# Kernel optimization log

Hardware: AMD Instinct MI355X
Metric: run time of the kernel (lower is better)

The kernel has to match this reference:

```python
import jax, jax.numpy as jnp
import numpy as np

HIDDEN = 4096       # in_features of gate/up proj
INTER = 11008       # intermediate_size (per projection)
GROUP = 128         # GPTQ group size
B, S = 4, 2048
NIB = jnp.uint32(0xF)


def _pack_rows(nib):
    """Pack 4-bit values along rows: [8*R, C] uint32 -> [R, C] uint32."""
    r = nib.reshape(-1, 8, nib.shape[-1])
    shifts = (jnp.arange(8, dtype=jnp.uint32) * 4)[None, :, None]
    return jnp.sum(r << shifts, axis=1, dtype=jnp.uint32)  # disjoint bits -> sum == OR


def _pack_cols(nib):
    """Pack 4-bit values along cols: [G, 8*C] uint32 -> [G, C] uint32."""
    r = nib.reshape(nib.shape[0], -1, 8)
    shifts = (jnp.arange(8, dtype=jnp.uint32) * 4)[None, None, :]
    return jnp.sum(r << shifts, axis=2, dtype=jnp.uint32)


def setup_inputs() -> dict:
    key = jax.random.key(0)
    ks = jax.random.split(key, 7)
    n_groups = HIDDEN // GROUP          # 32 groups for gate_up
    n_groups_d = INTER // GROUP         # 86 groups for down

    x = jax.random.normal(ks[0], (B, S, HIDDEN), jnp.float32)

    # gate_up_proj: in=HIDDEN, out=2*INTER
    nib_w_gu = jax.random.randint(ks[1], (HIDDEN, 2 * INTER), 0, 16).astype(jnp.uint32)
    nib_z_gu = jax.random.randint(ks[2], (n_groups, 2 * INTER), 0, 15).astype(jnp.uint32)
    qweight_gu = _pack_rows(nib_w_gu)                          # [HIDDEN//8, 2*INTER]
    qzeros_gu = _pack_cols(nib_z_gu)                           # [n_groups, 2*INTER//8]
    scales_gu = jax.random.uniform(ks[3], (n_groups, 2 * INTER), jnp.float32, 0.005, 0.02)
    g_idx_gu = (jnp.arange(HIDDEN, dtype=jnp.int32) // GROUP)

    # down_proj: in=INTER, out=HIDDEN
    nib_w_d = jax.random.randint(ks[4], (INTER, HIDDEN), 0, 16).astype(jnp.uint32)
    nib_z_d = jax.random.randint(ks[5], (n_groups_d, HIDDEN), 0, 15).astype(jnp.uint32)
    qweight_down = _pack_rows(nib_w_d)                         # [INTER//8, HIDDEN]
    qzeros_down = _pack_cols(nib_z_d)                          # [n_groups_d, HIDDEN//8]
    scales_down = jax.random.uniform(ks[6], (n_groups_d, HIDDEN), jnp.float32, 0.005, 0.02)
    g_idx_down = (jnp.arange(INTER, dtype=jnp.int32) // GROUP)

    return {
        "x": x,
        "qweight_gu": qweight_gu, "qzeros_gu": qzeros_gu,
        "scales_gu": scales_gu, "g_idx_gu": g_idx_gu,
        "qweight_down": qweight_down, "qzeros_down": qzeros_down,
        "scales_down": scales_down, "g_idx_down": g_idx_down,
    }


def _dequant(qw, qz, sc, g_idx):
    """GPTQ v2 dequant: W[i,j] = sc[g[i],j] * (wq[i,j] - (zq[g[i],j] + 1))."""
    shifts = jnp.arange(8, dtype=jnp.uint32) * 4
    # unpack qweight along rows: [R, C] -> [8*R, C]
    wq = ((qw[:, None, :] >> shifts[None, :, None]) & NIB)
    wq = wq.reshape(-1, qw.shape[1]).astype(jnp.float32)
    # unpack qzeros along cols: [G, C//8] -> [G, C]; +1 per GPTQ v2 convention
    zq = ((qz[:, :, None] >> shifts[None, None, :]) & NIB)
    zq = zq.reshape(qz.shape[0], -1).astype(jnp.float32) + 1.0
    return sc[g_idx] * (wq - zq[g_idx])  # [in, out]


def reference(x, qweight_gu, qzeros_gu, scales_gu, g_idx_gu,
              qweight_down, qzeros_down, scales_down, g_idx_down):
    w_gu = _dequant(qweight_gu, qzeros_gu, scales_gu, g_idx_gu)          # [HIDDEN, 2*INTER]
    inter = jnp.einsum('bsh,hf->bsf', x, w_gu)                            # [B,S,2*INTER]
    gate, up = inter[..., :INTER], inter[..., INTER:]
    h = jax.nn.silu(gate) * up                                            # SwiGLU
    w_d = _dequant(qweight_down, qzeros_down, scales_down, g_idx_down)   # [INTER, HIDDEN]
    return jnp.einsum('bsf,fh->bsh', h, w_d)
```

## Files before the change

kernel.cpp:

```cpp
#include <hip/hip_runtime.h>
#include <stdint.h>

#define HIDDEN 4096
#define INTER  11008
#define NTOK   8192
#define WROW   22016

typedef __bf16 bf16;
typedef __bf16 bf16x8 __attribute__((ext_vector_type(8)));
typedef _Float16 f16;
typedef _Float16 f16x2 __attribute__((ext_vector_type(2)));
typedef _Float16 f16x8 __attribute__((ext_vector_type(8)));
typedef float  f32x4  __attribute__((ext_vector_type(4)));
typedef unsigned int u32x4 __attribute__((ext_vector_type(4)));

__device__ __forceinline__ void gload16(const void* g, void* l) {
  __builtin_amdgcn_global_load_lds(
      (const __attribute__((address_space(1))) void*)g,
      (__attribute__((address_space(3))) void*)l, 16, 0, 0);
}
__device__ __forceinline__ void gload4(const void* g, void* l) {
  __builtin_amdgcn_global_load_lds(
      (const __attribute__((address_space(1))) void*)g,
      (__attribute__((address_space(3))) void*)l, 4, 0, 0);
}

__global__ __launch_bounds__(256) void cvt_f16_kernel(const float* __restrict__ x,
                                                      f16* __restrict__ y) {
  const int i = (blockIdx.x * 256 + threadIdx.x) * 8;
  f32x4 a = *(const f32x4*)(x + i);
  f32x4 b = *(const f32x4*)(x + i + 4);
  f16x8 v;
#pragma unroll
  for (int j = 0; j < 4; ++j) { v[2 * j] = (f16)a[j]; v[2 * j + 1] = (f16)b[j]; }
  *(f16x8*)(y + i) = v;
}

__global__ __launch_bounds__(256) void spak_kernel(const uint32_t* __restrict__ qz,
                                                   const float* __restrict__ sc,
                                                   uint32_t* __restrict__ outp) {
  const int idx = blockIdx.x * 256 + threadIdx.x;
  const int gq = idx / WROW;
  const int n = idx - gq * WROW;
  const int grp = n >> 5, win = n & 31;
  const int jg = (win < 16) ? grp * 16 + win : INTER + grp * 16 + (win - 16);
  const float s = sc[(size_t)gq * WROW + jg];
  const uint32_t z = (qz[(size_t)gq * (WROW / 8) + (jg >> 3)] >> ((jg & 7) * 4)) & 15u;
  union { f16 h[2]; uint32_t u; } a, b;
  a.h[0] = (f16)s; a.h[1] = (f16)s;
  b.h[0] = (f16)(float)(1025u + z); b.h[1] = b.h[0];
  outp[(size_t)idx * 2 + 0] = a.u;
  outp[(size_t)idx * 2 + 1] = b.u;
}

__global__ __launch_bounds__(256) void repackB_kernel(const uint32_t* __restrict__ qw,
                                                      uint32_t* __restrict__ outp) {
  const size_t idx = (size_t)blockIdx.x * 256 + threadIdx.x;
  const int c = (int)(idx & 2047);
  const int kt = (int)((idx >> 11) & 63);
  const int nb = (int)(idx >> 17);
  const int j = c & 3;
  const int chunk = c >> 2;
  const int r = chunk >> 6;
  const int wc = (chunk >> 4) & 3;
  const int fr = chunk & 15;
  const int col = wc * 32 + fr + (j & 1) * 16 + (j >> 1) * 128;
  const int n = nb * 256 + col;
  const int grp = n >> 5, win = n & 31;
  const int jg = (win < 16) ? grp * 16 + win : INTER + grp * 16 + (win - 16);
  outp[idx] = qw[(size_t)(kt * 8 + r) * WROW + jg];
}

__global__ __launch_bounds__(256) void dequant_kernel(const uint32_t* __restrict__ qw,
                                                      const uint32_t* __restrict__ qz,
                                                      const float* __restrict__ sc,
                                                      bf16* __restrict__ out,
                                                      int J, int Kout) {
  __shared__ __align__(16) bf16 T[64 * 256];
  const int tid = threadIdx.x;
  const int tx = tid & 63, ty = tid >> 6;
  const int j0 = blockIdx.x * 64, r0 = blockIdx.y * 32;
  const int j = j0 + tx;
  const int J8 = J >> 3;
#pragma unroll
  for (int i = 0; i < 8; ++i) {
    const int r = r0 + ty * 8 + i;
    const int g = r >> 4;
    const uint32_t w = qw[(size_t)r * J + j];
    const float s = sc[(size_t)g * J + j];
    const uint32_t zb = (qz[(size_t)g * J8 + (j >> 3)] >> ((j & 7) * 4)) & 15u;
    const float zoff = (float)(zb + 1u);
    bf16x8 v;
#pragma unroll
    for (int e = 0; e < 8; ++e) {
      const float wv = (float)((w >> (e * 4)) & 15u);
      v[e] = (bf16)(s * (wv - zoff));
    }
    const int lb = (tx * 512 + (ty * 8 + i) * 16) ^ ((tx & 31) << 4);
    *(bf16x8*)((char*)T + lb) = v;
  }
  __syncthreads();
#pragma unroll
  for (int u = 0; u < 8; ++u) {
    const int unit = u * 256 + tid;
    const int jj = unit >> 5;
    const int ob = (unit & 31) * 16;
    const int lb = (jj * 512 + ob) ^ ((jj & 31) << 4);
    bf16x8 v = *(const bf16x8*)((const char*)T + lb);
    *(bf16x8*)(out + (size_t)(j0 + jj) * Kout + r0 * 8 + (ob >> 1)) = v;
  }
}

#define OFF_BP 65536
#define OFF_SPK 81920

#define BAR __builtin_amdgcn_s_barrier()
#define LGKM0                                              \
  do {                                                     \
    asm volatile("s_waitcnt lgkmcnt(0)" ::: "memory");     \
    __builtin_amdgcn_sched_barrier(0);                     \
  } while (0)
#define VM2 asm volatile("s_waitcnt vmcnt(2)" ::: "memory")
#define VM3 asm volatile("s_waitcnt vmcnt(3)" ::: "memory")

#define STG_A(buf, h, tt)                                                      \
  do {                                                                         \
    gload16(sA00 + ((size_t)((h) * 128) * (HIDDEN * 2)) + (size_t)(tt) * 128,  \
            lds + (buf) * 32768 + (h) * 16384 + w * 1024);                     \
    gload16(sA00 + ((size_t)((h) * 128 + 64) * (HIDDEN * 2)) + (size_t)(tt) * 128, \
            lds + (buf) * 32768 + (h) * 16384 + 8192 + w * 1024);              \
  } while (0)

#define STG_B(buf, tt)                                                         \
  gload16(repk_src + (size_t)(tt) * 2048 + tid * 4,                            \
          lds + OFF_BP + (buf) * 8192 + tid * 16)

#define STG_SPK(gt)                                                           \
  gload4(spakg + ((size_t)(gt) * WROW + n0) * 2 + tid,                        \
         lds + OFF_SPK + ((gt) & 3) * 2048 + w * 256)

__device__ __forceinline__ f16x8 unpack8s(uint32_t u, f16x2 s2, f16x2 k2) {
  const uint32_t MSK = 0x000F000Fu, M = 0x64006400u;
  uint32_t q0 = (u & MSK) | M;
  uint32_t q1 = ((u >> 4) & MSK) | M;
  uint32_t q2 = ((u >> 8) & MSK) | M;
  uint32_t q3 = ((u >> 12) & MSK) | M;
  f16x2 w0 = (__builtin_bit_cast(f16x2, q0) - k2) * s2;
  f16x2 w1 = (__builtin_bit_cast(f16x2, q1) - k2) * s2;
  f16x2 w2 = (__builtin_bit_cast(f16x2, q2) - k2) * s2;
  f16x2 w3 = (__builtin_bit_cast(f16x2, q3) - k2) * s2;
  f16x8 r;
  r[0] = w0[0]; r[1] = w0[1]; r[2] = w1[0]; r[3] = w1[1];
  r[4] = w2[0]; r[5] = w2[1]; r[6] = w3[0]; r[7] = w3[1];
  return r;
}

#define UNP_SL(AVH, BUIDX, NH, NJ, KK, R, C)                                   \
  do {                                                                         \
    bv[NJ][KK] = unpack8s(bu[BUIDX], s2r[NH][NJ], k2r[NH][NJ]);                \
    _Pragma("unroll") for (int mi = 0; mi < 4; ++mi)                           \
      acc[(R) + mi][C] = __builtin_amdgcn_mfma_f32_16x16x32_f16(               \
          AVH[mi][KK], bv[NJ][KK], acc[(R) + mi][C], 0, 0, 0);                 \
  } while (0)

#define MFMA16(AVH, R, CBASE)                                                  \
  do {                                                                         \
    _Pragma("unroll") for (int kk = 0; kk < 2; ++kk)                           \
      _Pragma("unroll") for (int nj = 0; nj < 2; ++nj)                         \
        _Pragma("unroll") for (int mi = 0; mi < 4; ++mi)                       \
          acc[(R) + mi][(CBASE) + nj] = __builtin_amdgcn_mfma_f32_16x16x32_f16(\
              AVH[mi][kk], bv[nj][kk], acc[(R) + mi][(CBASE) + nj], 0, 0, 0);  \
  } while (0)

__global__ __launch_bounds__(512, 2) void gemm1q(const f16* __restrict__ A,
                                                 const uint32_t* __restrict__ repk,
                                                 const uint32_t* __restrict__ spakg,
                                                 bf16* __restrict__ H) {
  extern __shared__ char lds[];
  const int tid = threadIdx.x;
  const int lane = tid & 63, w = tid >> 6;
  const int wr = w >> 2, wc = w & 3;
  const int fr = lane & 15, fg = lane >> 4;
  constexpr int NT = HIDDEN / 64;

  const int wg = blockIdx.x;
  const int nb = wg % (WROW / 256), mb = wg / (WROW / 256);
  const int m0 = mb << 8, n0 = nb << 8;

  const int rbase = tid >> 3;
  const int cbyte0 = (tid & 7) * 16;
  const int cL0 = cbyte0 ^ ((rbase & 7) << 4);
  const char* sA00 = (const char*)A + (size_t)(m0 + rbase) * (size_t)(HIDDEN * 2) + cL0;

  const uint32_t* repk_src = repk + (size_t)nb * 64 * 2048;

  const int swz = (fr & 7) << 4;
  const int ck[2] = {(fg * 16) ^ swz, (64 + fg * 16) ^ swz};
  const int aro = (wr * 64 + fr) * 128;
  auto lda = [&](int buf, int mh, int mi, int kk) -> f16x8 {
    return *(const f16x8*)(lds + buf * 32768 + mh * 16384 + aro + mi * 2048 + ck[kk]);
  };
  const int c1b = ((fg * 4 + wc) * 16 + fr) * 16;
  const int ncol[2][2] = {{wc * 32 + fr, wc * 32 + 16 + fr},
                          {wc * 32 + 128 + fr, wc * 32 + 144 + fr}};

  f32x4 acc[8][4];
#pragma unroll
  for (int i = 0; i < 8; ++i)
#pragma unroll
    for (int j = 0; j < 4; ++j) acc[i][j] = (f32x4)0.0f;
  f16x8 av0[4][2], av1[4][2], bv[2][2];
  uint32_t bu[8];
  f16x2 s2r[2][2], k2r[2][2];

  STG_SPK(0);
  STG_A(0, 0, 0);
  STG_B(0, 0);
  STG_A(0, 1, 0);
  VM2;
  BAR;

  for (int t = 0; t < NT; ++t) {
    const int cb = t & 1, nx = cb ^ 1, g = t >> 1;
    const int t1 = (t + 1 < NT) ? t + 1 : 0;

#pragma unroll
    for (int mi = 0; mi < 4; ++mi) { av0[mi][0] = lda(cb, 0, mi, 0); av0[mi][1] = lda(cb, 0, mi, 1); }
    {
      u32x4 v1 = *(const u32x4*)(lds + OFF_BP + cb * 8192 + c1b);
      u32x4 v2 = *(const u32x4*)(lds + OFF_BP + cb * 8192 + c1b + 4096);
      bu[0] = v1.x; bu[1] = v2.x; bu[2] = v1.y; bu[3] = v2.y;
      bu[4] = v1.z; bu[5] = v2.z; bu[6] = v1.w; bu[7] = v2.w;
    }
    if ((t & 1) == 0) {
      const char* sp = lds + OFF_SPK + (g & 3) * 2048;
#pragma unroll
      for (int nh = 0; nh < 2; ++nh)
#pragma unroll
        for (int nj = 0; nj < 2; ++nj) {
          s2r[nh][nj] = *(const f16x2*)(sp + ncol[nh][nj] * 8);
          k2r[nh][nj] = *(const f16x2*)(sp + ncol[nh][nj] * 8 + 4);
        }
    }
    STG_A(nx, 0, t1);
    STG_B(nx, t1);
    VM3;
    BAR; LGKM0;
    __builtin_amdgcn_s_setprio(1);
    UNP_SL(av0, 0, 0, 0, 0, 0, 0);
    UNP_SL(av0, 1, 0, 0, 1, 0, 0);
    UNP_SL(av0, 2, 0, 1, 0, 0, 1);
    UNP_SL(av0, 3, 0, 1, 1, 0, 1);
    __builtin_amdgcn_s_setprio(0);
    __builtin_amdgcn_sched_barrier(0);
    BAR;

#pragma unroll
    for (int mi = 0; mi < 4; ++mi) { av1[mi][0] = lda(cb, 1, mi, 0); av1[mi][1] = lda(cb, 1, mi, 1); }
    if (t & 1) {
      const int gt = (g + 1 < 32) ? g + 1 : 31;
      STG_SPK(gt);
    }
    STG_A(nx, 1, t1);
    BAR; LGKM0;
    __builtin_amdgcn_s_setprio(1);
    MFMA16(av1, 4, 0);
    __builtin_amdgcn_s_setprio(0);
    __builtin_amdgcn_sched_barrier(0);
    BAR;

    __builtin_amdgcn_s_setprio(1);
    UNP_SL(av1, 4, 1, 0, 0, 4, 2);
    UNP_SL(av1, 5, 1, 0, 1, 4, 2);
    UNP_SL(av1, 6, 1, 1, 0, 4, 3);
    UNP_SL(av1, 7, 1, 1, 1, 4, 3);
    MFMA16(av0, 0, 2);
    __builtin_amdgcn_s_setprio(0);
    __builtin_amdgcn_sched_barrier(0);
    VM2;
    BAR;
  }
  asm volatile("s_waitcnt vmcnt(0)" ::: "memory");

#pragma unroll
  for (int mh = 0; mh < 2; ++mh)
#pragma unroll
    for (int mi = 0; mi < 4; ++mi)
#pragma unroll
      for (int nh = 0; nh < 2; ++nh) {
        const f32x4 gv4 = acc[mh * 4 + mi][nh * 2];
        const f32x4 uv4 = acc[mh * 4 + mi][nh * 2 + 1];
        const int col = (n0 >> 1) + wc * 16 + nh * 64 + fr;
#pragma unroll
        for (int rr = 0; rr < 4; ++rr) {
          const int row = m0 + wr * 64 + mh * 128 + mi * 16 + fg * 4 + rr;
          const float gv = gv4[rr], uv = uv4[rr];
          H[(size_t)row * INTER + col] = (bf16)(gv / (1.0f + __expf(-gv)) * uv);
        }
      }
}

#define OFF_A2 0
#define OFF_B2 32768

#define STG2(mat, buf, h, t)                                                   \
  do {                                                                         \
    gload16(s##mat[h][0] + (size_t)(t) * 128,                                  \
            lds + (buf) * 65536 + OFF_##mat + (h) * 16384 + w * 1024);         \
    gload16(s##mat[h][1] + (size_t)(t) * 128,                                  \
            lds + (buf) * 65536 + OFF_##mat + (h) * 16384 + 8192 + w * 1024);  \
  } while (0)
#define VM6 asm volatile("s_waitcnt vmcnt(6)" ::: "memory")

#define MFMA_Q2(MH, NH)                                                        \
  do {                                                                         \
    __builtin_amdgcn_s_setprio(1);                                             \
    _Pragma("unroll") for (int kk = 0; kk < 2; ++kk) {                         \
      _Pragma("unroll") for (int nj = 0; nj < 2; ++nj) {                       \
        _Pragma("unroll") for (int mi = 0; mi < 4; ++mi) {                     \
          acc[(MH)*4 + mi][(NH)*2 + nj] = __builtin_amdgcn_mfma_f32_16x16x32_bf16( \
              av[mi][kk], bv[nj][kk], acc[(MH)*4 + mi][(NH)*2 + nj], 0, 0, 0); \
        }                                                                      \
      }                                                                        \
    }                                                                          \
    __builtin_amdgcn_s_setprio(0);                                             \
    __builtin_amdgcn_sched_barrier(0);                                         \
  } while (0)

template <int K, int NT, int NNB>
__global__ __launch_bounds__(512, 2) void gemm8p(const bf16* __restrict__ A,
                                                 const bf16* __restrict__ Bm,
                                                 float* __restrict__ O) {
  extern __shared__ char lds[];
  const int tid = threadIdx.x;
  const int lane = tid & 63, w = tid >> 6;
  const int wr = w >> 2, wc = w & 3;
  const int fr = lane & 15, fg = lane >> 4;

  const int wg = blockIdx.x;
  const int nb = wg % NNB, mb = wg / NNB;
  const int m0 = mb << 8, n0 = nb << 8;

  const char* sA2[2][2];
  const char* sB2[2][2];
#pragma unroll
  for (int h = 0; h < 2; ++h)
#pragma unroll
    for (int l = 0; l < 2; ++l) {
      const int d = h * 16384 + (l * 512 + tid) * 16;
      const int r = d >> 7;
      const int cL = (d & 127) ^ ((r & 7) << 4);
      sA2[h][l] = (const char*)A + (size_t)(m0 + r) * (size_t)(K * 2) + cL;
      sB2[h][l] = (const char*)Bm + (size_t)(n0 + r) * (size_t)(K * 2) + cL;
    }

  const int swz = (fr & 7) << 4;
  const int ck[2] = {(fg * 16) ^ swz, (64 + fg * 16) ^ swz};
  const int aro = (wr * 64 + fr) * 128;
  const int bro = OFF_B2 + (wc * 32 + fr) * 128;

  auto lda = [&](int buf, int mh, int mi, int kk) -> bf16x8 {
    return *(const bf16x8*)(lds + buf * 65536 + mh * 16384 + aro + mi * 2048 + ck[kk]);
  };
  auto ldb = [&](int buf, int nh, int nj, int kk) -> bf16x8 {
    return *(const bf16x8*)(lds + buf * 65536 + bro + nh * 16384 + nj * 2048 + ck[kk]);
  };

  f32x4 acc[8][4];
#pragma unroll
  for (int i = 0; i < 8; ++i)
#pragma unroll
    for (int j = 0; j < 4; ++j) acc[i][j] = (f32x4)0.0f;
  bf16x8 av[4][2], bv[2][2];

  STG2(A2, 0, 0, 0);
  STG2(B2, 0, 0, 0);
  STG2(B2, 0, 1, 0);
  STG2(A2, 0, 1, 0);
  STG2(A2, 1, 0, 1);
  STG2(B2, 1, 1, 1);
  STG2(A2, 1, 1, 1);
  VM6;
  BAR;

  for (int t = 0; t < NT; ++t) {
    const int cb = t & 1, nx = cb ^ 1;
    const int t1 = (t + 1 < NT) ? t + 1 : 0;
    const int t2 = (t + 2 < NT) ? t + 2 : 0;

#pragma unroll
    for (int mi = 0; mi < 4; ++mi) { av[mi][0] = lda(cb, 0, mi, 0); av[mi][1] = lda(cb, 0, mi, 1); }
#pragma unroll
    for (int nj = 0; nj < 2; ++nj) { bv[nj][0] = ldb(cb, 0, nj, 0); bv[nj][1] = ldb(cb, 0, nj, 1); }
    STG2(B2, nx, 0, t1);
    BAR; LGKM0;
    MFMA_Q2(0, 0);
    BAR;

#pragma unroll
    for (int nj = 0; nj < 2; ++nj) { bv[nj][0] = ldb(cb, 1, nj, 0); bv[nj][1] = ldb(cb, 1, nj, 1); }
    STG2(A2, cb, 0, t2);
    BAR; LGKM0;
    MFMA_Q2(0, 1);
    BAR;

#pragma unroll
    for (int mi = 0; mi < 4; ++mi) { av[mi][0] = lda(cb, 1, mi, 0); av[mi][1] = lda(cb, 1, mi, 1); }
    STG2(B2, cb, 1, t2);
    BAR; LGKM0;
    MFMA_Q2(1, 1);
    BAR;

#pragma unroll
    for (int nj = 0; nj < 2; ++nj) { bv[nj][0] = ldb(cb, 0, nj, 0); bv[nj][1] = ldb(cb, 0, nj, 1); }
    STG2(A2, cb, 1, t2);
    VM6;
    BAR; LGKM0;
    MFMA_Q2(1, 0);
    BAR;
  }

#pragma unroll
  for (int mh = 0; mh < 2; ++mh)
#pragma unroll
    for (int mi = 0; mi < 4; ++mi)
#pragma unroll
      for (int nh = 0; nh < 2; ++nh)
#pragma unroll
        for (int nj = 0; nj < 2; ++nj) {
          const f32x4 a = acc[mh * 4 + mi][nh * 2 + nj];
          const int col = n0 + wc * 32 + nh * 128 + nj * 16 + fr;
#pragma unroll
          for (int rr = 0; rr < 4; ++rr) {
            const int row = m0 + wr * 64 + mh * 128 + mi * 16 + fg * 4 + rr;
            __builtin_nontemporal_store(a[rr], &O[(size_t)row * HIDDEN + col]);
          }
        }
}

extern "C" void kernel_launch(void* const* d_in, const int* in_sizes, int n_in,
                              void* d_out, int out_size, void* d_ws, size_t ws_size,
                              hipStream_t stream) {
  (void)in_sizes; (void)n_in; (void)out_size; (void)ws_size;
  const float*    x     = (const float*)d_in[0];
  const uint32_t* qw_gu = (const uint32_t*)d_in[1];
  const uint32_t* qz_gu = (const uint32_t*)d_in[2];
  const float*    sc_gu = (const float*)d_in[3];
  const uint32_t* qw_d  = (const uint32_t*)d_in[5];
  const uint32_t* qz_d  = (const uint32_t*)d_in[6];
  const float*    sc_d  = (const float*)d_in[7];
  float*          out   = (float*)d_out;

  char* ws = (char*)d_ws;
  const size_t XB  = (size_t)NTOK * HIDDEN * 2;
  const size_t W2B = (size_t)HIDDEN * INTER * 2;
  const size_t HB  = (size_t)NTOK * INTER * 2;
  const size_t SPB = (size_t)32 * WROW * 2 * 4;
  f16*      xb    = (f16*)ws;
  bf16*     wt    = (bf16*)(ws + XB);
  bf16*     hb    = (bf16*)(ws + XB + W2B);
  uint32_t* spakg = (uint32_t*)(ws + XB + W2B + HB);
  uint32_t* repk  = (uint32_t*)(ws + XB + W2B + HB + SPB);

  hipFuncSetAttribute((const void*)&gemm1q,
                      hipFuncAttributeMaxDynamicSharedMemorySize, 90112);
  hipFuncSetAttribute((const void*)&gemm8p<INTER, INTER / 64, HIDDEN / 256>,
                      hipFuncAttributeMaxDynamicSharedMemorySize, 131072);

  cvt_f16_kernel<<<NTOK * HIDDEN / 2048, 256, 0, stream>>>(x, xb);
  spak_kernel<<<32 * WROW / 256, 256, 0, stream>>>(qz_gu, sc_gu, spakg);
  repackB_kernel<<<((WROW / 256) * 64 * 2048) / 256, 256, 0, stream>>>(qw_gu, repk);

  gemm1q<<<(WROW / 256) * (NTOK / 256), 512, 90112, stream>>>(xb, repk, spakg, hb);

  dequant_kernel<<<dim3(HIDDEN / 64, (INTER / 8) / 32), 256, 0, stream>>>(
      qw_d, qz_d, sc_d, wt, HIDDEN, INTER);
  gemm8p<INTER, INTER / 64, HIDDEN / 256>
      <<<(HIDDEN / 256) * (NTOK / 256), 512, 131072, stream>>>(hb, wt, out);
}
```

Baseline: 2.113 ms.

## Restructure gemm1q inner loop to dequantize all B fragments up front and share one A register set

The per-tile schedule is reorganized so all eight B words are dequantized in the first phase against the first A half. The second A half then reuses the same av registers for all remaining MFMAs, which merges the last two phases into one and drops one barrier per iteration. This removes the separate av0/av1 and bu register arrays, lowering register pressure under the 512x2 launch bounds. In exchange, dequant work is no longer interleaved across phases, which may reduce overlap with MFMA, and more B fragment registers stay live.

```diff
diff --git a/kernel.cpp b/kernel.cpp
--- a/kernel.cpp
+++ b/kernel.cpp
@@ -155,21 +155,12 @@
   return r;
 }
 
-#define UNP_SL(AVH, BUIDX, NH, NJ, KK, R, C)                                   \
+#define UNP_SL(BV, WORD, NH, NJ, KK, C)                                        \
   do {                                                                         \
-    bv[NJ][KK] = unpack8s(bu[BUIDX], s2r[NH][NJ], k2r[NH][NJ]);                \
+    BV[NJ][KK] = unpack8s(WORD, s2r[NH][NJ], k2r[NH][NJ]);                     \
     _Pragma("unroll") for (int mi = 0; mi < 4; ++mi)                           \
-      acc[(R) + mi][C] = __builtin_amdgcn_mfma_f32_16x16x32_f16(               \
-          AVH[mi][KK], bv[NJ][KK], acc[(R) + mi][C], 0, 0, 0);                 \
-  } while (0)
-
-#define MFMA16(AVH, R, CBASE)                                                  \
-  do {                                                                         \
-    _Pragma("unroll") for (int kk = 0; kk < 2; ++kk)                           \
-      _Pragma("unroll") for (int nj = 0; nj < 2; ++nj)                         \
-        _Pragma("unroll") for (int mi = 0; mi < 4; ++mi)                       \
-          acc[(R) + mi][(CBASE) + nj] = __builtin_amdgcn_mfma_f32_16x16x32_f16(\
-              AVH[mi][kk], bv[nj][kk], acc[(R) + mi][(CBASE) + nj], 0, 0, 0);  \
+      acc[mi][C] = __builtin_amdgcn_mfma_f32_16x16x32_f16(                     \
+          av[mi][KK], BV[NJ][KK], acc[mi][C], 0, 0, 0);                        \
   } while (0)
 
 __global__ __launch_bounds__(512, 2) void gemm1q(const f16* __restrict__ A,
@@ -209,8 +200,7 @@
   for (int i = 0; i < 8; ++i)
 #pragma unroll
     for (int j = 0; j < 4; ++j) acc[i][j] = (f32x4)0.0f;
-  f16x8 av0[4][2], av1[4][2], bv[2][2];
-  uint32_t bu[8];
+  f16x8 av[4][2], bv[2][2], bv2[2][2];
   f16x2 s2r[2][2], k2r[2][2];
 
   STG_SPK(0);
@@ -225,13 +215,9 @@
     const int t1 = (t + 1 < NT) ? t + 1 : 0;
 
 #pragma unroll
-    for (int mi = 0; mi < 4; ++mi) { av0[mi][0] = lda(cb, 0, mi, 0); av0[mi][1] = lda(cb, 0, mi, 1); }
-    {
-      u32x4 v1 = *(const u32x4*)(lds + OFF_BP + cb * 8192 + c1b);
-      u32x4 v2 = *(const u32x4*)(lds + OFF_BP + cb * 8192 + c1b + 4096);
-      bu[0] = v1.x; bu[1] = v2.x; bu[2] = v1.y; bu[3] = v2.y;
-      bu[4] = v1.z; bu[5] = v2.z; bu[6] = v1.w; bu[7] = v2.w;
-    }
+    for (int mi = 0; mi < 4; ++mi) { av[mi][0] = lda(cb, 0, mi, 0); av[mi][1] = lda(cb, 0, mi, 1); }
+    u32x4 v1 = *(const u32x4*)(lds + OFF_BP + cb * 8192 + c1b);
+    u32x4 v2 = *(const u32x4*)(lds + OFF_BP + cb * 8192 + c1b + 4096);
     if ((t & 1) == 0) {
       const char* sp = lds + OFF_SPK + (g & 3) * 2048;
 #pragma unroll
@@ -247,16 +233,20 @@
     VM3;
     BAR; LGKM0;
     __builtin_amdgcn_s_setprio(1);
-    UNP_SL(av0, 0, 0, 0, 0, 0, 0);
-    UNP_SL(av0, 1, 0, 0, 1, 0, 0);
-    UNP_SL(av0, 2, 0, 1, 0, 0, 1);
-    UNP_SL(av0, 3, 0, 1, 1, 0, 1);
+    UNP_SL(bv,  v1.x, 0, 0, 0, 0);
+    UNP_SL(bv,  v2.x, 0, 0, 1, 0);
+    UNP_SL(bv,  v1.y, 0, 1, 0, 1);
+    UNP_SL(bv,  v2.y, 0, 1, 1, 1);
+    UNP_SL(bv2, v1.z, 1, 0, 0, 2);
+    UNP_SL(bv2, v2.z, 1, 0, 1, 2);
+    UNP_SL(bv2, v1.w, 1, 1, 0, 3);
+    UNP_SL(bv2, v2.w, 1, 1, 1, 3);
     __builtin_amdgcn_s_setprio(0);
     __builtin_amdgcn_sched_barrier(0);
     BAR;
 
 #pragma unroll
-    for (int mi = 0; mi < 4; ++mi) { av1[mi][0] = lda(cb, 1, mi, 0); av1[mi][1] = lda(cb, 1, mi, 1); }
+    for (int mi = 0; mi < 4; ++mi) { av[mi][0] = lda(cb, 1, mi, 0); av[mi][1] = lda(cb, 1, mi, 1); }
     if (t & 1) {
       const int gt = (g + 1 < 32) ? g + 1 : 31;
       STG_SPK(gt);
@@ -264,17 +254,19 @@
     STG_A(nx, 1, t1);
     BAR; LGKM0;
     __builtin_amdgcn_s_setprio(1);
-    MFMA16(av1, 4, 0);
-    __builtin_amdgcn_s_setprio(0);
-    __builtin_amdgcn_sched_barrier(0);
-    BAR;
-
-    __builtin_amdgcn_s_setprio(1);
-    UNP_SL(av1, 4, 1, 0, 0, 4, 2);
-    UNP_SL(av1, 5, 1, 0, 1, 4, 2);
-    UNP_SL(av1, 6, 1, 1, 0, 4, 3);
-    UNP_SL(av1, 7, 1, 1, 1, 4, 3);
-    MFMA16(av0, 0, 2);
+#pragma unroll
+    for (int kk = 0; kk < 2; ++kk)
+#pragma unroll
+      for (int nj = 0; nj < 2; ++nj) {
+#pragma unroll
+        for (int mi = 0; mi < 4; ++mi)
+          acc[4 + mi][nj] = __builtin_amdgcn_mfma_f32_16x16x32_f16(
+              av[mi][kk], bv[nj][kk], acc[4 + mi][nj], 0, 0, 0);
+#pragma unroll
+        for (int mi = 0; mi < 4; ++mi)
+          acc[4 + mi][2 + nj] = __builtin_amdgcn_mfma_f32_16x16x32_f16(
+              av[mi][kk], bv2[nj][kk], acc[4 + mi][2 + nj], 0, 0, 0);
+      }
     __builtin_amdgcn_s_setprio(0);
     __builtin_amdgcn_sched_barrier(0);
     VM2;
```

Result: no change. 2.085 ms (-1.3%).
